# Kernel tuning notes

Hardware: AMD Instinct MI355X
Metric: run time of the kernel (lower is better)

## Reference

```python
import jax, jax.numpy as jnp
import numpy as np
import math

B, S, H, NH, NB = 2, 512, 128, 4, 2
D = H // NH
V_ITEMS, NCAT, NMETA, BAG, TSPAN = 50000, 1000, 16, 5, 256
EPS_EMB, EPS = 1e-5, 1e-8
NEG = -(2.0 ** 32) + 1.0


def _ln(x, g, b, eps):
    m = x.mean(-1, keepdims=True)
    v = ((x - m) ** 2).mean(-1, keepdims=True)
    return (x - m) / jnp.sqrt(v + eps) * g + b


def setup_inputs() -> dict:
    key = jax.random.key(0)
    ks = jax.random.split(key, 24)
    sc = 0.02
    inp = {}
    inp['input_ids'] = jax.random.randint(ks[0], (B, S), 0, V_ITEMS + 1)
    inp['metadata_seq'] = jax.random.normal(ks[1], (B, S, NMETA), jnp.float32)
    inp['category_seq'] = jax.random.randint(ks[2], (B, S, BAG), 0, NCAT + 1)
    inp['time_matrix'] = jax.random.randint(ks[3], (B, S, S), 0, TSPAN + 1)
    item = jax.random.normal(ks[4], (V_ITEMS + 1, H), jnp.float32) * sc
    inp['item_emb_w'] = item.at[0].set(0.0)  # padding_idx=0 cleared
    cat = jax.random.normal(ks[5], (NCAT + 1, H // 2), jnp.float32) * sc
    inp['cat_emb_w'] = cat.at[0].set(0.0)
    inp['num_W'] = jax.random.normal(ks[6], (H // 2, NMETA), jnp.float32) * sc
    inp['num_b'] = jnp.zeros((H // 2,), jnp.float32)
    inp['fusion_W'] = jax.random.normal(ks[7], (H, 2 * H), jnp.float32) * sc
    inp['fusion_b'] = jnp.zeros((H,), jnp.float32)
    inp['emb_ln_g'] = jnp.ones((H,), jnp.float32)
    inp['emb_ln_b'] = jnp.zeros((H,), jnp.float32)
    inp['pos_K_w'] = jax.random.normal(ks[8], (S, H), jnp.float32) * sc
    inp['pos_V_w'] = jax.random.normal(ks[9], (S, H), jnp.float32) * sc
    inp['time_K_w'] = jax.random.normal(ks[10], (TSPAN + 1, H), jnp.float32) * sc
    inp['time_V_w'] = jax.random.normal(ks[11], (TSPAN + 1, H), jnp.float32) * sc
    inp['attn_ln_g'] = jnp.ones((NB, H), jnp.float32)
    inp['attn_ln_b'] = jnp.zeros((NB, H), jnp.float32)
    inp['Q_W'] = jax.random.normal(ks[12], (NB, H, H), jnp.float32) * sc
    inp['Q_b'] = jnp.zeros((NB, H), jnp.float32)
    inp['K_W'] = jax.random.normal(ks[13], (NB, H, H), jnp.float32) * sc
    inp['K_b'] = jnp.zeros((NB, H), jnp.float32)
    inp['V_W'] = jax.random.normal(ks[14], (NB, H, H), jnp.float32) * sc
    inp['V_b'] = jnp.zeros((NB, H), jnp.float32)
    inp['fwd_ln_g'] = jnp.ones((NB, H), jnp.float32)
    inp['fwd_ln_b'] = jnp.zeros((NB, H), jnp.float32)
    inp['w1_W'] = jax.random.normal(ks[15], (NB, H, H), jnp.float32) * sc
    inp['w1_b'] = jnp.zeros((NB, H), jnp.float32)
    inp['w2_W'] = jax.random.normal(ks[16], (NB, H, H), jnp.float32) * sc
    inp['w2_b'] = jnp.zeros((NB, H), jnp.float32)
    inp['last_ln_g'] = jnp.ones((H,), jnp.float32)
    inp['last_ln_b'] = jnp.zeros((H,), jnp.float32)
    return inp


def reference(input_ids, metadata_seq, category_seq, time_matrix, item_emb_w,
              cat_emb_w, num_W, num_b, fusion_W, fusion_b, emb_ln_g, emb_ln_b,
              pos_K_w, pos_V_w, time_K_w, time_V_w, attn_ln_g, attn_ln_b,
              Q_W, Q_b, K_W, K_b, V_W, V_b, fwd_ln_g, fwd_ln_b,
              w1_W, w1_b, w2_W, w2_b, last_ln_g, last_ln_b):
    # ---- seq2vec ----
    item_v = item_emb_w[input_ids] * math.sqrt(H)            # [B,S,H]
    bag_mask = (category_seq != 0)                           # EmbeddingBag mean, padding_idx=0
    cat_e = cat_emb_w[category_seq] * bag_mask[..., None]    # [B,S,BAG,H/2]
    cat_v = cat_e.sum(-2) / jnp.maximum(bag_mask.sum(-1, keepdims=True), 1)
    num_v = metadata_seq @ num_W.T + num_b                   # [B,S,H/2]
    comb = jnp.concatenate([item_v, num_v, cat_v], axis=-1)  # [B,S,2H]
    vecs = _ln(comb @ fusion_W.T + fusion_b, emb_ln_g, emb_ln_b, EPS_EMB)

    # ---- vec2feats ----
    posK = pos_K_w.reshape(S, NH, D)
    posV = pos_V_w.reshape(S, NH, D)
    tK = time_K_w[time_matrix].reshape(B, S, S, NH, D)       # [B,S,S,h,d]
    tV = time_V_w[time_matrix].reshape(B, S, S, NH, D)
    timeline = (input_ids == 0)                              # [B,S]
    keep = (~timeline)[..., None].astype(vecs.dtype)
    vecs = vecs * keep
    causal = ~jnp.tril(jnp.ones((S, S), bool))               # mask where j > i
    inv_sqrt_d = 1.0 / math.sqrt(D)

    for i in range(NB):
        Qn = _ln(vecs, attn_ln_g[i], attn_ln_b[i], EPS)
        Q = (Qn @ Q_W[i].T + Q_b[i]).reshape(B, S, NH, D)
        K = (vecs @ K_W[i].T + K_b[i]).reshape(B, S, NH, D)
        V = (vecs @ V_W[i].T + V_b[i]).reshape(B, S, NH, D)
        aw = jnp.einsum('bihd,bjhd->bhij', Q, K)
        aw = aw + jnp.einsum('bihd,jhd->bhij', Q, posK)
        aw = aw + jnp.einsum('bijhd,bihd->bhij', tK, Q)
        aw = aw * inv_sqrt_d
        aw = jnp.where(timeline[:, None, :, None], NEG, aw)  # masks query rows (as in torch)
        aw = jnp.where(causal[None, None], NEG, aw)
        aw = jax.nn.softmax(aw, axis=-1)
        out = jnp.einsum('bhij,bjhd->bihd', aw, V)
        out = out + jnp.einsum('bhij,jhd->bihd', aw, posV)
        out = out + jnp.einsum('bhij,bijhd->bihd', aw, tV)
        out = out.reshape(B, S, H)
        vecs = Qn + out
        vecs = _ln(vecs, fwd_ln_g[i], fwd_ln_b[i], EPS)
        h1 = jax.nn.gelu(vecs @ w1_W[i].T + w1_b[i], approximate=False)
        vecs = vecs + (h1 @ w2_W[i].T + w2_b[i])
        vecs = vecs * keep

    return _ln(vecs, last_ln_g, last_ln_b, EPS)
```

## Files before the change

### kernel.cpp

```cpp
#include <hip/hip_runtime.h>
#include <math.h>

#define Bn 2
#define Sn 512
#define Hn 128
#define NHn 4
#define Dn 32
#define BAGn 5
#define NMETAn 16
#define ROWS 1024
#define NBn 2
#define Tt 257

#define NEGF (-4294967295.0f)
#define INV_SQRT_D 0.17677669529663687f
#define SQRT_H 11.313708498984761f
#define EPS_EMB 1e-5f
#define EPSF 1e-8f

#define OFF_QN    0
#define OFF_Q     131072
#define OFF_K     262144
#define OFF_V     393216
#define OFF_O     524288

static __device__ __forceinline__ float red64(float v) {
#pragma unroll
    for (int m = 1; m < 64; m <<= 1) v += __shfl_xor(v, m, 64);
    return v;
}
static __device__ __forceinline__ float red64max(float v) {
#pragma unroll
    for (int m = 1; m < 64; m <<= 1) v = fmaxf(v, __shfl_xor(v, m, 64));
    return v;
}
static __device__ __forceinline__ float dot4(float4 a, float4 b) {
    return a.x * b.x + a.y * b.y + a.z * b.z + a.w * b.w;
}
static __device__ __forceinline__ float red4(float v) {
    v += __shfl_xor(v, 1, 64);
    v += __shfl_xor(v, 2, 64);
    return v;
}

__global__ __launch_bounds__(256) void embed_qkv_kernel(
    const int* __restrict__ ids, const float* __restrict__ meta,
    const int* __restrict__ cats,
    const float* __restrict__ item_w, const float* __restrict__ cat_w,
    const float* __restrict__ numW, const float* __restrict__ numb,
    const float* __restrict__ fusW, const float* __restrict__ fusb,
    const float* __restrict__ elng, const float* __restrict__ elnb,
    const float* __restrict__ alng, const float* __restrict__ alnb,
    const float* __restrict__ QW, const float* __restrict__ Qb,
    const float* __restrict__ KW, const float* __restrict__ Kb,
    const float* __restrict__ VW, const float* __restrict__ Vb,
    const float* __restrict__ posK, const float* __restrict__ posV,
    float* __restrict__ Qn, float* __restrict__ Q,
    float* __restrict__ K, float* __restrict__ V)
{
    int r0 = blockIdx.x * 2, t = threadIdx.x;
    __shared__ __align__(16) float combs[512];
    __shared__ __align__(16) float xs[256];
    __shared__ __align__(16) float qs[256];
    __shared__ float wsum[8];
    __shared__ int idl[2];
    if (t < 2) idl[t] = ids[r0 + t];
    __syncthreads();
    { int r = t >> 7, c = t & 127; combs[r * 256 + c] = item_w[idl[r] * Hn + c] * SQRT_H; }
    if (t < 128) {
        int r = t >> 6, c = t & 63;
        const float4* m4 = (const float4*)(meta + (r0 + r) * NMETAn);
        const float4* w4 = (const float4*)(numW + c * NMETAn);
        float acc = numb[c];
#pragma unroll
        for (int j = 0; j < 4; ++j) acc += dot4(m4[j], w4[j]);
        combs[r * 256 + 128 + c] = acc;
    } else {
        int u = t - 128, r = u >> 6, c = u & 63;
        float ca = 0.f; int cnt = 0;
#pragma unroll
        for (int k2 = 0; k2 < BAGn; ++k2) {
            int cc2 = cats[(r0 + r) * BAGn + k2];
            if (cc2 != 0) { ca += cat_w[cc2 * 64 + c]; cnt++; }
        }
        combs[r * 256 + 192 + c] = ca / (float)(cnt > 0 ? cnt : 1);
    }
    __syncthreads();

    int q = t & 3, g = t >> 2;
#pragma unroll
    for (int p = 0; p < 2; ++p) {
        int h = p * 64 + g;
        const float4* w4 = (const float4*)(fusW + h * 256) + q;
        const float4* c0 = (const float4*)(combs) + q;
        const float4* c1 = (const float4*)(combs + 256) + q;
        float a0 = 0.f, a1 = 0.f;
#pragma unroll
        for (int j = 0; j < 16; ++j) {
            float4 w = w4[j * 4];
            a0 += dot4(c0[j * 4], w);
            a1 += dot4(c1[j * 4], w);
        }
        a0 = red4(a0); a1 = red4(a1);
        if (q == 0)      xs[h]       = a0 + fusb[h];
        else if (q == 1) xs[128 + h] = a1 + fusb[h];
    }
    __syncthreads();

    int w_ = t >> 6, row = w_ >> 1, l = t & 63, ch = ((w_ & 1) << 6) + l;
    float x = xs[row * 128 + ch];
    float s1 = red64(x);
    if (l == 0) wsum[w_] = s1;
    __syncthreads();
    float mean = (wsum[row * 2] + wsum[row * 2 + 1]) * (1.f / 128.f);
    float dlt = x - mean;
    float s2 = red64(dlt * dlt);
    if (l == 0) wsum[4 + w_] = s2;
    __syncthreads();
    float rstd = rsqrtf((wsum[4 + row * 2] + wsum[4 + row * 2 + 1]) * (1.f / 128.f) + EPS_EMB);
    float xv = dlt * rstd * elng[ch] + elnb[ch];
    xv = (idl[row] == 0) ? 0.f : xv;
    __syncthreads();
    xs[row * 128 + ch] = xv;
    __syncthreads();
    s1 = red64(xv);
    if (l == 0) wsum[w_] = s1;
    __syncthreads();
    mean = (wsum[row * 2] + wsum[row * 2 + 1]) * (1.f / 128.f);
    dlt = xv - mean;
    s2 = red64(dlt * dlt);
    if (l == 0) wsum[4 + w_] = s2;
    __syncthreads();
    rstd = rsqrtf((wsum[4 + row * 2] + wsum[4 + row * 2 + 1]) * (1.f / 128.f) + EPSF);
    float qn = dlt * rstd * alng[ch] + alnb[ch];
    qs[row * 128 + ch] = qn;
    Qn[(r0 + row) * 128 + ch] = qn;
    __syncthreads();

#pragma unroll
    for (int p = 0; p < 2; ++p) {
        int h = p * 64 + g;
        const float4* qw = (const float4*)(QW + h * 128) + q;
        const float4* kw = (const float4*)(KW + h * 128) + q;
        const float4* vw = (const float4*)(VW + h * 128) + q;
        const float4* s0p = (const float4*)(qs) + q;
        const float4* s1p = (const float4*)(qs + 128) + q;
        const float4* x0p = (const float4*)(xs) + q;
        const float4* x1p = (const float4*)(xs + 128) + q;
        float aq0 = 0, aq1 = 0, ak0 = 0, ak1 = 0, av0 = 0, av1 = 0;
#pragma unroll
        for (int j = 0; j < 8; ++j) {
            float4 wq = qw[j * 4], wk = kw[j * 4], wv = vw[j * 4];
            float4 u0 = s0p[j * 4], u1 = s1p[j * 4];
            float4 y0 = x0p[j * 4], y1 = x1p[j * 4];
            aq0 += dot4(u0, wq); aq1 += dot4(u1, wq);
            ak0 += dot4(y0, wk); ak1 += dot4(y1, wk);
            av0 += dot4(y0, wv); av1 += dot4(y1, wv);
        }
        aq0 = red4(aq0); aq1 = red4(aq1);
        ak0 = red4(ak0); ak1 = red4(ak1);
        av0 = red4(av0); av1 = red4(av1);
        if (q == 0) {
            int si = r0 & (Sn - 1);
            Q[r0 * Hn + h] = aq0 + Qb[h];
            K[r0 * Hn + h] = ak0 + Kb[h] + posK[si * Hn + h];
            V[r0 * Hn + h] = av0 + Vb[h] + posV[si * Hn + h];
        } else if (q == 1) {
            int si = (r0 + 1) & (Sn - 1);
            Q[(r0 + 1) * Hn + h] = aq1 + Qb[h];
            K[(r0 + 1) * Hn + h] = ak1 + Kb[h] + posK[si * Hn + h];
            V[(r0 + 1) * Hn + h] = av1 + Vb[h] + posV[si * Hn + h];
        }
    }
}

static __device__ __forceinline__ void attn_phase(
    int b, int h, int i0, int t,
    const int* __restrict__ ids, const int* __restrict__ tmat,
    const float* __restrict__ Q, const float* __restrict__ K,
    const float* __restrict__ V,
    const float* __restrict__ tKw, const float* __restrict__ tVw,
    float* __restrict__ O,
    float* Kt, float* Vt, float* Stile, int* trowT,
    float* QTl, float* ql, int* tlf)
{
    if (t < 4) tlf[t] = (ids[b * Sn + i0 + t] == 0) ? 1 : 0;
    if (t < 128) {
        int q_ = t >> 5, d = t & 31;
        ql[q_ * 33 + d] = Q[(b * Sn + i0 + q_) * Hn + h * 32 + d];
    }
    __syncthreads();

    for (int tt = t; tt < Tt; tt += 256) {
        const float4* tk4 = (const float4*)(tKw + tt * Hn + h * 32);
        float a0 = 0.f, a1 = 0.f, a2 = 0.f, a3 = 0.f;
#pragma unroll
        for (int dv = 0; dv < 8; ++dv) {
            float4 w4 = tk4[dv];
            int d = dv * 4;
            a0 += ql[d] * w4.x + ql[d + 1] * w4.y + ql[d + 2] * w4.z + ql[d + 3] * w4.w;
            a1 += ql[33 + d] * w4.x + ql[34 + d] * w4.y + ql[35 + d] * w4.z + ql[36 + d] * w4.w;
            a2 += ql[66 + d] * w4.x + ql[67 + d] * w4.y + ql[68 + d] * w4.z + ql[69 + d] * w4.w;
            a3 += ql[99 + d] * w4.x + ql[100 + d] * w4.y + ql[101 + d] * w4.z + ql[102 + d] * w4.w;
        }
        QTl[tt] = a0; QTl[260 + tt] = a1; QTl[520 + tt] = a2; QTl[780 + tt] = a3;
    }

    int tl_any = tlf[0] | tlf[1] | tlf[2] | tlf[3];
    int ntiles = tl_any ? 8 : ((i0 + 3) >> 6) + 1;

    int iq = t >> 6, jj = t & 63;
    int i_g = i0 + iq;
    int my_tl = tlf[iq];
    const int* trow = tmat + (b * Sn + i_g) * Sn;

    float qreg[32];
#pragma unroll
    for (int d = 0; d < 32; ++d) qreg[d] = ql[iq * 33 + d];

    int jq = jj >> 5, d = jj & 31;
    float m = -INFINITY, lsum = 0.f, acc = 0.f;

    for (int jt = 0; jt < ntiles; ++jt) {
        int j0 = jt * 64;
        __syncthreads();
        for (int f = t; f < 64 * 8; f += 256) {
            int jl = f >> 3, dv = f & 7;
            const float* src = K + (b * Sn + j0 + jl) * Hn + h * 32 + dv * 4;
            float4 w4 = *(const float4*)src;
            float* kd = &Kt[jl * 33 + dv * 4];
            kd[0] = w4.x; kd[1] = w4.y; kd[2] = w4.z; kd[3] = w4.w;
            float4 v4 = *(const float4*)(V + (b * Sn + j0 + jl) * Hn + h * 32 + dv * 4);
            float* vd = &Vt[jl * 33 + dv * 4];
            vd[0] = v4.x; vd[1] = v4.y; vd[2] = v4.z; vd[3] = v4.w;
        }
        __syncthreads();

        int active = my_tl || (j0 <= i_g);
        if (active) {
            int j = j0 + jj;
            float sv = NEGF;
            int tv = trow[j];
            if (!my_tl && j <= i_g) {
                float a = 0.f;
#pragma unroll
                for (int dd = 0; dd < 32; ++dd)
                    a += qreg[dd] * Kt[jj * 33 + dd];
                sv = (a + QTl[iq * 260 + tv]) * INV_SQRT_D;
            }
            float mt = red64max(sv);
            float mnew = fmaxf(m, mt);
            float alpha = expf(m - mnew);
            float p = expf(sv - mnew);
            lsum = lsum * alpha + red64(p);
            m = mnew;
            acc *= alpha;
            Stile[iq * 64 + jj] = p;
            trowT[iq * 64 + jj] = tv;
        }
        __syncthreads();
        if (active) {
            int base = jq * 32;
#pragma unroll 8
            for (int jl = base; jl < base + 32; ++jl) {
                float pp = Stile[iq * 64 + jl];
                int tv2 = trowT[iq * 64 + jl];
                acc += pp * (Vt[jl * 33 + d] + tVw[tv2 * Hn + h * 32 + d]);
            }
        }
    }

    float a2 = acc + __shfl_xor(acc, 32, 64);
    if (jj < 32)
        O[(b * Sn + i_g) * Hn + h * 32 + d] = a2 / lsum;
}

__global__ __launch_bounds__(256) void attn_kernel(
    const int* ids, const int* tmat,
    const float* Q, const float* K, const float* V,
    const float* tKw, const float* tVw, float* O)
{
    __shared__ float Kt[64 * 33];
    __shared__ float Vt[64 * 33];
    __shared__ float Stile[4 * 64];
    __shared__ int   trowT[4 * 64];
    __shared__ float QTl[4 * 260];
    __shared__ float ql[4 * 33];
    __shared__ int tlf[4];
    int blk = blockIdx.x, t = threadIdx.x;
    int bh = blk & 7;
    int s  = blk >> 3;
    int g = s >> 5, r = s & 31;
    int mm;
    if      (g == 0) mm = r;
    else if (g == 1) mm = 127 - r;
    else if (g == 2) mm = 32 + r;
    else             mm = 95 - r;
    int b = bh >> 2, h = bh & 3;
    attn_phase(b, h, mm * 4, t, ids, tmat, Q, K, V, tKw, tVw, O,
               Kt, Vt, Stile, trowT, QTl, ql, tlf);
}

__global__ __launch_bounds__(256) void ffn_qkv_kernel(
    const int* __restrict__ ids, float* __restrict__ Qn,
    const float* __restrict__ O,
    const float* __restrict__ flng, const float* __restrict__ flnb,
    const float* __restrict__ w1W, const float* __restrict__ w1b,
    const float* __restrict__ w2W, const float* __restrict__ w2b,
    const float* __restrict__ alng, const float* __restrict__ alnb,
    const float* __restrict__ QW, const float* __restrict__ Qb,
    const float* __restrict__ KW, const float* __restrict__ Kb,
    const float* __restrict__ VW, const float* __restrict__ Vb,
    const float* __restrict__ posK, const float* __restrict__ posV,
    float* __restrict__ Q, float* __restrict__ K, float* __restrict__ V,
    const float* __restrict__ llng, const float* __restrict__ llnb,
    float* __restrict__ out, int nb, int last)
{
    int r0 = blockIdx.x * 2, t = threadIdx.x;
    __shared__ __align__(16) float ys[256];
    __shared__ __align__(16) float h1s[256];
    __shared__ float wsum[8];
    int id0 = ids[r0], id1 = ids[r0 + 1];

    ys[t] = Qn[r0 * 128 + t] + O[r0 * 128 + t];
    __syncthreads();
    int w_ = t >> 6, row = w_ >> 1, l = t & 63, ch = ((w_ & 1) << 6) + l;
    float x = ys[row * 128 + ch];
    float s1 = red64(x);
    if (l == 0) wsum[w_] = s1;
    __syncthreads();
    float mean = (wsum[row * 2] + wsum[row * 2 + 1]) * (1.f / 128.f);
    float dlt = x - mean;
    float s2 = red64(dlt * dlt);
    if (l == 0) wsum[4 + w_] = s2;
    __syncthreads();
    float rstd = rsqrtf((wsum[4 + row * 2] + wsum[4 + row * 2 + 1]) * (1.f / 128.f) + EPSF);
    float yv = dlt * rstd * flng[nb * 128 + ch] + flnb[nb * 128 + ch];
    __syncthreads();
    ys[row * 128 + ch] = yv;
    __syncthreads();

    int q = t & 3, g = t >> 2;
#pragma unroll
    for (int p = 0; p < 2; ++p) {
        int h = p * 64 + g;
        const float4* w4 = (const float4*)(w1W + nb * 16384 + h * 128) + q;
        const float4* y0 = (const float4*)(ys) + q;
        const float4* y1 = (const float4*)(ys + 128) + q;
        float a0 = 0.f, a1 = 0.f;
#pragma unroll
        for (int j = 0; j < 8; ++j) {
            float4 w = w4[j * 4];
            a0 += dot4(y0[j * 4], w);
            a1 += dot4(y1[j * 4], w);
        }
        a0 = red4(a0); a1 = red4(a1);
        if (q == 0) {
            float v0 = a0 + w1b[nb * 128 + h];
            h1s[h] = 0.5f * v0 * (1.f + erff(v0 * 0.70710678118654752f));
        } else if (q == 1) {
            float v1 = a1 + w1b[nb * 128 + h];
            h1s[128 + h] = 0.5f * v1 * (1.f + erff(v1 * 0.70710678118654752f));
        }
    }
    __syncthreads();

    float z00, z01, z10, z11;
    {
        float zz[2][2];
#pragma unroll
        for (int p = 0; p < 2; ++p) {
            int h = p * 64 + g;
            const float4* w4 = (const float4*)(w2W + nb * 16384 + h * 128) + q;
            const float4* y0 = (const float4*)(h1s) + q;
            const float4* y1 = (const float4*)(h1s + 128) + q;
            float a0 = 0.f, a1 = 0.f;
#pragma unroll
            for (int j = 0; j < 8; ++j) {
                float4 w = w4[j * 4];
                a0 += dot4(y0[j * 4], w);
                a1 += dot4(y1[j * 4], w);
            }
            a0 = red4(a0); a1 = red4(a1);
            float b_ = w2b[nb * 128 + h];
            zz[p][0] = (id0 == 0) ? 0.f : (a0 + b_ + ys[h]);
            zz[p][1] = (id1 == 0) ? 0.f : (a1 + b_ + ys[128 + h]);
        }
        z00 = zz[0][0]; z10 = zz[1][0]; z01 = zz[0][1]; z11 = zz[1][1];
    }
    __syncthreads();
    if (q == 0)      { h1s[g] = z00;        h1s[64 + g] = z10; }
    else if (q == 1) { h1s[128 + g] = z01;  h1s[192 + g] = z11; }
    __syncthreads();

    if (last) {
        x = h1s[row * 128 + ch];
        s1 = red64(x);
        if (l == 0) wsum[w_] = s1;
        __syncthreads();
        mean = (wsum[row * 2] + wsum[row * 2 + 1]) * (1.f / 128.f);
        dlt = x - mean;
        s2 = red64(dlt * dlt);
        if (l == 0) wsum[4 + w_] = s2;
        __syncthreads();
        rstd = rsqrtf((wsum[4 + row * 2] + wsum[4 + row * 2 + 1]) * (1.f / 128.f) + EPSF);
        out[(r0 + row) * 128 + ch] = dlt * rstd * llng[ch] + llnb[ch];
        return;
    }

    int nq = nb + 1;
    x = h1s[row * 128 + ch];
    s1 = red64(x);
    if (l == 0) wsum[w_] = s1;
    __syncthreads();
    mean = (wsum[row * 2] + wsum[row * 2 + 1]) * (1.f / 128.f);
    dlt = x - mean;
    s2 = red64(dlt * dlt);
    if (l == 0) wsum[4 + w_] = s2;
    __syncthreads();
    rstd = rsqrtf((wsum[4 + row * 2] + wsum[4 + row * 2 + 1]) * (1.f / 128.f) + EPSF);
    float qn = dlt * rstd * alng[nq * 128 + ch] + alnb[nq * 128 + ch];
    __syncthreads();
    ys[row * 128 + ch] = qn;
    Qn[(r0 + row) * 128 + ch] = qn;
    __syncthreads();

#pragma unroll
    for (int p = 0; p < 2; ++p) {
        int h = p * 64 + g;
        const float4* qw = (const float4*)(QW + nq * 16384 + h * 128) + q;
        const float4* kw = (const float4*)(KW + nq * 16384 + h * 128) + q;
        const float4* vw = (const float4*)(VW + nq * 16384 + h * 128) + q;
        const float4* s0p = (const float4*)(ys) + q;
        const float4* s1p = (const float4*)(ys + 128) + q;
        const float4* x0p = (const float4*)(h1s) + q;
        const float4* x1p = (const float4*)(h1s + 128) + q;
        float aq0 = 0, aq1 = 0, ak0 = 0, ak1 = 0, av0 = 0, av1 = 0;
#pragma unroll
        for (int j = 0; j < 8; ++j) {
            float4 wq = qw[j * 4], wk = kw[j * 4], wv = vw[j * 4];
            float4 u0 = s0p[j * 4], u1 = s1p[j * 4];
            float4 y0 = x0p[j * 4], y1 = x1p[j * 4];
            aq0 += dot4(u0, wq); aq1 += dot4(u1, wq);
            ak0 += dot4(y0, wk); ak1 += dot4(y1, wk);
            av0 += dot4(y0, wv); av1 += dot4(y1, wv);
        }
        aq0 = red4(aq0); aq1 = red4(aq1);
        ak0 = red4(ak0); ak1 = red4(ak1);
        av0 = red4(av0); av1 = red4(av1);
        if (q == 0) {
            int si = r0 & (Sn - 1);
            Q[r0 * Hn + h] = aq0 + Qb[nq * 128 + h];
            K[r0 * Hn + h] = ak0 + Kb[nq * 128 + h] + posK[si * Hn + h];
            V[r0 * Hn + h] = av0 + Vb[nq * 128 + h] + posV[si * Hn + h];
        } else if (q == 1) {
            int si = (r0 + 1) & (Sn - 1);
            Q[(r0 + 1) * Hn + h] = aq1 + Qb[nq * 128 + h];
            K[(r0 + 1) * Hn + h] = ak1 + Kb[nq * 128 + h] + posK[si * Hn + h];
            V[(r0 + 1) * Hn + h] = av1 + Vb[nq * 128 + h] + posV[si * Hn + h];
        }
    }
}

extern "C" void kernel_launch(void* const* d_in, const int* in_sizes, int n_in,
                              void* d_out, int out_size, void* d_ws, size_t ws_size,
                              hipStream_t stream) {
    const int*   ids   = (const int*)  d_in[0];
    const float* meta  = (const float*)d_in[1];
    const int*   cats  = (const int*)  d_in[2];
    const int*   tmat  = (const int*)  d_in[3];
    const float* itemw = (const float*)d_in[4];
    const float* catw  = (const float*)d_in[5];
    const float* numW  = (const float*)d_in[6];
    const float* numb  = (const float*)d_in[7];
    const float* fusW  = (const float*)d_in[8];
    const float* fusb  = (const float*)d_in[9];
    const float* elng  = (const float*)d_in[10];
    const float* elnb  = (const float*)d_in[11];
    const float* posK  = (const float*)d_in[12];
    const float* posV  = (const float*)d_in[13];
    const float* tKw   = (const float*)d_in[14];
    const float* tVw   = (const float*)d_in[15];
    const float* alng  = (const float*)d_in[16];
    const float* alnb  = (const float*)d_in[17];
    const float* QW    = (const float*)d_in[18];
    const float* Qb    = (const float*)d_in[19];
    const float* KW    = (const float*)d_in[20];
    const float* Kb    = (const float*)d_in[21];
    const float* VW    = (const float*)d_in[22];
    const float* Vb    = (const float*)d_in[23];
    const float* flng  = (const float*)d_in[24];
    const float* flnb  = (const float*)d_in[25];
    const float* w1W   = (const float*)d_in[26];
    const float* w1b   = (const float*)d_in[27];
    const float* w2W   = (const float*)d_in[28];
    const float* w2b   = (const float*)d_in[29];
    const float* llng  = (const float*)d_in[30];
    const float* llnb  = (const float*)d_in[31];
    (void)in_sizes; (void)n_in; (void)out_size; (void)ws_size;

    float* ws = (float*)d_ws;
    float* Qnp = ws + OFF_QN;
    float* Qp  = ws + OFF_Q;
    float* Kp  = ws + OFF_K;
    float* Vp  = ws + OFF_V;
    float* Op  = ws + OFF_O;
    float* outp = (float*)d_out;

    embed_qkv_kernel<<<ROWS / 2, 256, 0, stream>>>(
        ids, meta, cats, itemw, catw, numW, numb, fusW, fusb, elng, elnb,
        alng, alnb, QW, Qb, KW, Kb, VW, Vb, posK, posV, Qnp, Qp, Kp, Vp);
    for (int nb = 0; nb < NBn; ++nb) {
        attn_kernel<<<1024, 256, 0, stream>>>(ids, tmat, Qp, Kp, Vp, tKw, tVw, Op);
        ffn_qkv_kernel<<<ROWS / 2, 256, 0, stream>>>(
            ids, Qnp, Op, flng, flnb, w1W, w1b, w2W, w2b,
            alng, alnb, QW, Qb, KW, Kb, VW, Vb, posK, posV,
            Qp, Kp, Vp, llng, llnb, outp, nb, (nb == NBn - 1) ? 1 : 0);
    }
}
```

Before: 229.0 us.

## Prefetch time matrix and time tables into cache; parallelize QT projection

The embedding kernel now reads the whole time matrix and both time embedding tables and throws the values away, so they sit in L2/MALL before the attention kernels run. An empty asm statement keeps the dead loads from being removed. The attention kernel's per-query time-key projection now splits each 32-wide dot product across 4 lanes with shuffle reductions, so all 256 threads share the 257 time buckets instead of one thread per bucket looping serially. The cost is extra memory traffic in the embedding kernel and some additional shuffle instructions.

```diff
diff --git a/kernel.cpp b/kernel.cpp
--- a/kernel.cpp
+++ b/kernel.cpp
@@ -55,6 +55,8 @@
     const float* __restrict__ KW, const float* __restrict__ Kb,
     const float* __restrict__ VW, const float* __restrict__ Vb,
     const float* __restrict__ posK, const float* __restrict__ posV,
+    const int* __restrict__ tmat, const float* __restrict__ tKw,
+    const float* __restrict__ tVw,
     float* __restrict__ Qn, float* __restrict__ Q,
     float* __restrict__ K, float* __restrict__ V)
 {
@@ -64,6 +66,20 @@
     __shared__ __align__(16) float qs[256];
     __shared__ float wsum[8];
     __shared__ int idl[2];
+
+    int pfi = 0; float pff = 0.f;
+    {
+        const int* tm = tmat + blockIdx.x * 1024;
+#pragma unroll
+        for (int j = 0; j < 4; ++j) pfi += tm[t + j * 256];
+        if (t < 64) {
+            int off = blockIdx.x * 64 + t;
+            pff = tKw[off] + tVw[off];
+        } else if (blockIdx.x == 0 && t < 192) {
+            pff = tKw[32704 + t] + tVw[32704 + t];
+        }
+    }
+
     if (t < 2) idl[t] = ids[r0 + t];
     __syncthreads();
     { int r = t >> 7, c = t & 127; combs[r * 256 + c] = item_w[idl[r] * Hn + c] * SQRT_H; }
@@ -85,6 +101,7 @@
         }
         combs[r * 256 + 192 + c] = ca / (float)(cnt > 0 ? cnt : 1);
     }
+    asm volatile("" :: "v"(pfi), "v"(pff));
     __syncthreads();
 
     int q = t & 3, g = t >> 2;
@@ -191,19 +208,48 @@
     }
     __syncthreads();
 
-    for (int tt = t; tt < Tt; tt += 256) {
-        const float4* tk4 = (const float4*)(tKw + tt * Hn + h * 32);
-        float a0 = 0.f, a1 = 0.f, a2 = 0.f, a3 = 0.f;
-#pragma unroll
-        for (int dv = 0; dv < 8; ++dv) {
-            float4 w4 = tk4[dv];
-            int d = dv * 4;
-            a0 += ql[d] * w4.x + ql[d + 1] * w4.y + ql[d + 2] * w4.z + ql[d + 3] * w4.w;
-            a1 += ql[33 + d] * w4.x + ql[34 + d] * w4.y + ql[35 + d] * w4.z + ql[36 + d] * w4.w;
-            a2 += ql[66 + d] * w4.x + ql[67 + d] * w4.y + ql[68 + d] * w4.z + ql[69 + d] * w4.w;
-            a3 += ql[99 + d] * w4.x + ql[100 + d] * w4.y + ql[101 + d] * w4.z + ql[102 + d] * w4.w;
-        }
-        QTl[tt] = a0; QTl[260 + tt] = a1; QTl[520 + tt] = a2; QTl[780 + tt] = a3;
+    {
+        int qq = t & 3, gg = t >> 2;
+#pragma unroll
+        for (int c = 0; c < 4; ++c) {
+            int tt = c * 64 + gg;
+            const float4* tk4 = (const float4*)(tKw + tt * Hn + h * 32);
+            float4 wA = tk4[qq];
+            float4 wB = tk4[qq + 4];
+            int dA = qq * 4, dB = 16 + qq * 4;
+            float a0 = ql[dA]*wA.x + ql[dA+1]*wA.y + ql[dA+2]*wA.z + ql[dA+3]*wA.w
+                     + ql[dB]*wB.x + ql[dB+1]*wB.y + ql[dB+2]*wB.z + ql[dB+3]*wB.w;
+            float a1 = ql[33+dA]*wA.x + ql[34+dA]*wA.y + ql[35+dA]*wA.z + ql[36+dA]*wA.w
+                     + ql[33+dB]*wB.x + ql[34+dB]*wB.y + ql[35+dB]*wB.z + ql[36+dB]*wB.w;
+            float a2 = ql[66+dA]*wA.x + ql[67+dA]*wA.y + ql[68+dA]*wA.z + ql[69+dA]*wA.w
+                     + ql[66+dB]*wB.x + ql[67+dB]*wB.y + ql[68+dB]*wB.z + ql[69+dB]*wB.w;
+            float a3 = ql[99+dA]*wA.x + ql[100+dA]*wA.y + ql[101+dA]*wA.z + ql[102+dA]*wA.w
+                     + ql[99+dB]*wB.x + ql[100+dB]*wB.y + ql[101+dB]*wB.z + ql[102+dB]*wB.w;
+            a0 = red4(a0); a1 = red4(a1); a2 = red4(a2); a3 = red4(a3);
+            if (qq == 0)      QTl[tt] = a0;
+            else if (qq == 1) QTl[260 + tt] = a1;
+            else if (qq == 2) QTl[520 + tt] = a2;
+            else              QTl[780 + tt] = a3;
+        }
+        if (t < 4) {
+            const float4* tk4 = (const float4*)(tKw + 256 * Hn + h * 32);
+            float4 wA = tk4[t];
+            float4 wB = tk4[t + 4];
+            int dA = t * 4, dB = 16 + t * 4;
+            float a0 = ql[dA]*wA.x + ql[dA+1]*wA.y + ql[dA+2]*wA.z + ql[dA+3]*wA.w
+                     + ql[dB]*wB.x + ql[dB+1]*wB.y + ql[dB+2]*wB.z + ql[dB+3]*wB.w;
+            float a1 = ql[33+dA]*wA.x + ql[34+dA]*wA.y + ql[35+dA]*wA.z + ql[36+dA]*wA.w
+                     + ql[33+dB]*wB.x + ql[34+dB]*wB.y + ql[35+dB]*wB.z + ql[36+dB]*wB.w;
+            float a2 = ql[66+dA]*wA.x + ql[67+dA]*wA.y + ql[68+dA]*wA.z + ql[69+dA]*wA.w
+                     + ql[66+dB]*wB.x + ql[67+dB]*wB.y + ql[68+dB]*wB.z + ql[69+dB]*wB.w;
+            float a3 = ql[99+dA]*wA.x + ql[100+dA]*wA.y + ql[101+dA]*wA.z + ql[102+dA]*wA.w
+                     + ql[99+dB]*wB.x + ql[100+dB]*wB.y + ql[101+dB]*wB.z + ql[102+dB]*wB.w;
+            a0 = red4(a0); a1 = red4(a1); a2 = red4(a2); a3 = red4(a3);
+            if (t == 0)      QTl[256] = a0;
+            else if (t == 1) QTl[516] = a1;
+            else if (t == 2) QTl[776] = a2;
+            else             QTl[1036] = a3;
+        }
     }
 
     int tl_any = tlf[0] | tlf[1] | tlf[2] | tlf[3];
@@ -509,7 +555,8 @@
 
     embed_qkv_kernel<<<ROWS / 2, 256, 0, stream>>>(
         ids, meta, cats, itemw, catw, numW, numb, fusW, fusb, elng, elnb,
-        alng, alnb, QW, Qb, KW, Kb, VW, Vb, posK, posV, Qnp, Qp, Kp, Vp);
+        alng, alnb, QW, Qb, KW, Kb, VW, Vb, posK, posV, tmat, tKw, tVw,
+        Qnp, Qp, Kp, Vp);
     for (int nb = 0; nb < NBn; ++nb) {
         attn_kernel<<<1024, 256, 0, stream>>>(ids, tmat, Qp, Kp, Vp, tKw, tVw, Op);
         ffn_qkv_kernel<<<ROWS / 2, 256, 0, stream>>>(
```

Result: faster. 224.2 us (-2.1%).

## Fuse attention with FFN/QKV per row pair and double-buffer K/V

Applied to the files above, without the earlier changes.

Attention and the following FFN/LayerNorm/next-QKV projection are merged into one kernel. Each block handles two query rows across all four heads, with 32-key tiles, 32-lane reductions, and V and tV read straight from global memory. K/V outputs now alternate between two workspace buffers, because other blocks still read the current K/V while the next ones are written. This drops the intermediate O buffer and two kernel launches. The embed kernel also touches time_matrix and the time embedding tables to warm the cache, at the cost of extra loads and fewer, heavier attention blocks.

```diff
diff --git a/kernel.cpp b/kernel.cpp
--- a/kernel.cpp
+++ b/kernel.cpp
@@ -20,18 +20,24 @@
 
 #define OFF_QN    0
 #define OFF_Q     131072
-#define OFF_K     262144
-#define OFF_V     393216
-#define OFF_O     524288
+#define OFF_K0    262144
+#define OFF_V0    393216
+#define OFF_K1    524288
+#define OFF_V1    655360
 
 static __device__ __forceinline__ float red64(float v) {
 #pragma unroll
     for (int m = 1; m < 64; m <<= 1) v += __shfl_xor(v, m, 64);
     return v;
 }
-static __device__ __forceinline__ float red64max(float v) {
-#pragma unroll
-    for (int m = 1; m < 64; m <<= 1) v = fmaxf(v, __shfl_xor(v, m, 64));
+static __device__ __forceinline__ float red32(float v) {
+#pragma unroll
+    for (int m = 1; m < 32; m <<= 1) v += __shfl_xor(v, m, 32);
+    return v;
+}
+static __device__ __forceinline__ float red32max(float v) {
+#pragma unroll
+    for (int m = 1; m < 32; m <<= 1) v = fmaxf(v, __shfl_xor(v, m, 32));
     return v;
 }
 static __device__ __forceinline__ float dot4(float4 a, float4 b) {
@@ -55,6 +61,8 @@
     const float* __restrict__ KW, const float* __restrict__ Kb,
     const float* __restrict__ VW, const float* __restrict__ Vb,
     const float* __restrict__ posK, const float* __restrict__ posV,
+    const int* __restrict__ tmat, const float* __restrict__ tKw,
+    const float* __restrict__ tVw,
     float* __restrict__ Qn, float* __restrict__ Q,
     float* __restrict__ K, float* __restrict__ V)
 {
@@ -64,6 +72,20 @@
     __shared__ __align__(16) float qs[256];
     __shared__ float wsum[8];
     __shared__ int idl[2];
+
+    int pfi = 0; float pff = 0.f;
+    {
+        const int* tm = tmat + blockIdx.x * 1024;
+#pragma unroll
+        for (int j = 0; j < 4; ++j) pfi += tm[t + j * 256];
+        if (t < 64) {
+            int off = blockIdx.x * 64 + t;
+            pff = tKw[off] + tVw[off];
+        } else if (blockIdx.x == 0 && t < 192) {
+            pff = tKw[32704 + t] + tVw[32704 + t];
+        }
+    }
+
     if (t < 2) idl[t] = ids[r0 + t];
     __syncthreads();
     { int r = t >> 7, c = t & 127; combs[r * 256 + c] = item_w[idl[r] * Hn + c] * SQRT_H; }
@@ -85,6 +107,7 @@
         }
         combs[r * 256 + 192 + c] = ca / (float)(cnt > 0 ? cnt : 1);
     }
+    asm volatile("" :: "v"(pfi), "v"(pff));
     __syncthreads();
 
     int q = t & 3, g = t >> 2;
@@ -174,136 +197,11 @@
     }
 }
 
-static __device__ __forceinline__ void attn_phase(
-    int b, int h, int i0, int t,
+__global__ __launch_bounds__(256) void attn_ffn_kernel(
     const int* __restrict__ ids, const int* __restrict__ tmat,
-    const float* __restrict__ Q, const float* __restrict__ K,
-    const float* __restrict__ V,
+    const float* Q, const float* K, const float* V,
     const float* __restrict__ tKw, const float* __restrict__ tVw,
-    float* __restrict__ O,
-    float* Kt, float* Vt, float* Stile, int* trowT,
-    float* QTl, float* ql, int* tlf)
-{
-    if (t < 4) tlf[t] = (ids[b * Sn + i0 + t] == 0) ? 1 : 0;
-    if (t < 128) {
-        int q_ = t >> 5, d = t & 31;
-        ql[q_ * 33 + d] = Q[(b * Sn + i0 + q_) * Hn + h * 32 + d];
-    }
-    __syncthreads();
-
-    for (int tt = t; tt < Tt; tt += 256) {
-        const float4* tk4 = (const float4*)(tKw + tt * Hn + h * 32);
-        float a0 = 0.f, a1 = 0.f, a2 = 0.f, a3 = 0.f;
-#pragma unroll
-        for (int dv = 0; dv < 8; ++dv) {
-            float4 w4 = tk4[dv];
-            int d = dv * 4;
-            a0 += ql[d] * w4.x + ql[d + 1] * w4.y + ql[d + 2] * w4.z + ql[d + 3] * w4.w;
-            a1 += ql[33 + d] * w4.x + ql[34 + d] * w4.y + ql[35 + d] * w4.z + ql[36 + d] * w4.w;
-            a2 += ql[66 + d] * w4.x + ql[67 + d] * w4.y + ql[68 + d] * w4.z + ql[69 + d] * w4.w;
-            a3 += ql[99 + d] * w4.x + ql[100 + d] * w4.y + ql[101 + d] * w4.z + ql[102 + d] * w4.w;
-        }
-        QTl[tt] = a0; QTl[260 + tt] = a1; QTl[520 + tt] = a2; QTl[780 + tt] = a3;
-    }
-
-    int tl_any = tlf[0] | tlf[1] | tlf[2] | tlf[3];
-    int ntiles = tl_any ? 8 : ((i0 + 3) >> 6) + 1;
-
-    int iq = t >> 6, jj = t & 63;
-    int i_g = i0 + iq;
-    int my_tl = tlf[iq];
-    const int* trow = tmat + (b * Sn + i_g) * Sn;
-
-    float qreg[32];
-#pragma unroll
-    for (int d = 0; d < 32; ++d) qreg[d] = ql[iq * 33 + d];
-
-    int jq = jj >> 5, d = jj & 31;
-    float m = -INFINITY, lsum = 0.f, acc = 0.f;
-
-    for (int jt = 0; jt < ntiles; ++jt) {
-        int j0 = jt * 64;
-        __syncthreads();
-        for (int f = t; f < 64 * 8; f += 256) {
-            int jl = f >> 3, dv = f & 7;
-            const float* src = K + (b * Sn + j0 + jl) * Hn + h * 32 + dv * 4;
-            float4 w4 = *(const float4*)src;
-            float* kd = &Kt[jl * 33 + dv * 4];
-            kd[0] = w4.x; kd[1] = w4.y; kd[2] = w4.z; kd[3] = w4.w;
-            float4 v4 = *(const float4*)(V + (b * Sn + j0 + jl) * Hn + h * 32 + dv * 4);
-            float* vd = &Vt[jl * 33 + dv * 4];
-            vd[0] = v4.x; vd[1] = v4.y; vd[2] = v4.z; vd[3] = v4.w;
-        }
-        __syncthreads();
-
-        int active = my_tl || (j0 <= i_g);
-        if (active) {
-            int j = j0 + jj;
-            float sv = NEGF;
-            int tv = trow[j];
-            if (!my_tl && j <= i_g) {
-                float a = 0.f;
-#pragma unroll
-                for (int dd = 0; dd < 32; ++dd)
-                    a += qreg[dd] * Kt[jj * 33 + dd];
-                sv = (a + QTl[iq * 260 + tv]) * INV_SQRT_D;
-            }
-            float mt = red64max(sv);
-            float mnew = fmaxf(m, mt);
-            float alpha = expf(m - mnew);
-            float p = expf(sv - mnew);
-            lsum = lsum * alpha + red64(p);
-            m = mnew;
-            acc *= alpha;
-            Stile[iq * 64 + jj] = p;
-            trowT[iq * 64 + jj] = tv;
-        }
-        __syncthreads();
-        if (active) {
-            int base = jq * 32;
-#pragma unroll 8
-            for (int jl = base; jl < base + 32; ++jl) {
-                float pp = Stile[iq * 64 + jl];
-                int tv2 = trowT[iq * 64 + jl];
-                acc += pp * (Vt[jl * 33 + d] + tVw[tv2 * Hn + h * 32 + d]);
-            }
-        }
-    }
-
-    float a2 = acc + __shfl_xor(acc, 32, 64);
-    if (jj < 32)
-        O[(b * Sn + i_g) * Hn + h * 32 + d] = a2 / lsum;
-}
-
-__global__ __launch_bounds__(256) void attn_kernel(
-    const int* ids, const int* tmat,
-    const float* Q, const float* K, const float* V,
-    const float* tKw, const float* tVw, float* O)
-{
-    __shared__ float Kt[64 * 33];
-    __shared__ float Vt[64 * 33];
-    __shared__ float Stile[4 * 64];
-    __shared__ int   trowT[4 * 64];
-    __shared__ float QTl[4 * 260];
-    __shared__ float ql[4 * 33];
-    __shared__ int tlf[4];
-    int blk = blockIdx.x, t = threadIdx.x;
-    int bh = blk & 7;
-    int s  = blk >> 3;
-    int g = s >> 5, r = s & 31;
-    int mm;
-    if      (g == 0) mm = r;
-    else if (g == 1) mm = 127 - r;
-    else if (g == 2) mm = 32 + r;
-    else             mm = 95 - r;
-    int b = bh >> 2, h = bh & 3;
-    attn_phase(b, h, mm * 4, t, ids, tmat, Q, K, V, tKw, tVw, O,
-               Kt, Vt, Stile, trowT, QTl, ql, tlf);
-}
-
-__global__ __launch_bounds__(256) void ffn_qkv_kernel(
-    const int* __restrict__ ids, float* __restrict__ Qn,
-    const float* __restrict__ O,
+    float* __restrict__ Qn,
     const float* __restrict__ flng, const float* __restrict__ flnb,
     const float* __restrict__ w1W, const float* __restrict__ w1b,
     const float* __restrict__ w2W, const float* __restrict__ w2b,
@@ -312,20 +210,132 @@
     const float* __restrict__ KW, const float* __restrict__ Kb,
     const float* __restrict__ VW, const float* __restrict__ Vb,
     const float* __restrict__ posK, const float* __restrict__ posV,
-    float* __restrict__ Q, float* __restrict__ K, float* __restrict__ V,
+    float* Qo, float* Ko, float* Vo,
     const float* __restrict__ llng, const float* __restrict__ llnb,
     float* __restrict__ out, int nb, int last)
 {
-    int r0 = blockIdx.x * 2, t = threadIdx.x;
-    __shared__ __align__(16) float ys[256];
-    __shared__ __align__(16) float h1s[256];
-    __shared__ float wsum[8];
+    __shared__ __align__(16) float sm[7722];
+    float* Kt    = sm;
+    float* QTl   = sm + 4608;
+    float* ql    = sm + 6688;
+    float* os    = sm + 6952;
+    float* Stile = sm + 7208;
+    int*   trowT = (int*)(sm + 7464);
+    int*   tlf   = (int*)(sm + 7720);
+
+    int blk = blockIdx.x, t = threadIdx.x;
+    int beta = blk & 1;
+    int m_ = blk >> 1;
+    int grp = (m_ < 128) ? m_ : 383 - m_;
+    int r0 = beta * Sn + grp * 2;
+
+    int w  = t >> 6;
+    int jj = t & 63;
+    int r  = jj >> 5;
+    int j  = jj & 31;
+
+    if (t < 2) tlf[t] = (ids[r0 + t] == 0) ? 1 : 0;
+    { int rr = t >> 7, d = t & 127; ql[rr * 132 + d] = Q[(r0 + rr) * Hn + d]; }
+    __syncthreads();
+
+    {
+        int q4 = t & 3, g4 = t >> 2;
+        const float4* ql0 = (const float4*)(ql);
+        const float4* ql1 = (const float4*)(ql + 132);
+#pragma unroll
+        for (int c = 0; c < 5; ++c) {
+            int tt = c * 64 + g4;
+            if (tt < Tt) {
+                const float4* tk = (const float4*)(tKw + tt * Hn);
+                float ah[4][2] = {{0.f,0.f},{0.f,0.f},{0.f,0.f},{0.f,0.f}};
+#pragma unroll
+                for (int cc = 0; cc < 8; ++cc) {
+                    int chn = cc * 4 + q4;
+                    float4 wv = tk[chn];
+                    ah[cc >> 1][0] += dot4(ql0[chn], wv);
+                    ah[cc >> 1][1] += dot4(ql1[chn], wv);
+                }
+#pragma unroll
+                for (int hh = 0; hh < 4; ++hh) {
+                    ah[hh][0] = red4(ah[hh][0]);
+                    ah[hh][1] = red4(ah[hh][1]);
+                }
+                if (q4 == 0)      { QTl[tt] = ah[0][0];        QTl[260 + tt] = ah[0][1]; }
+                else if (q4 == 1) { QTl[520 + tt] = ah[1][0];  QTl[780 + tt] = ah[1][1]; }
+                else if (q4 == 2) { QTl[1040 + tt] = ah[2][0]; QTl[1300 + tt] = ah[2][1]; }
+                else              { QTl[1560 + tt] = ah[3][0]; QTl[1820 + tt] = ah[3][1]; }
+            }
+        }
+    }
+
+    int tl_any = tlf[0] | tlf[1];
+    int my_tl = tlf[r];
+    int i_g = grp * 2 + r;
+    int ntiles = tl_any ? 16 : ((grp * 2 + 1) >> 5) + 1;
+    const int* trw = tmat + (size_t)(r0 + r) * Sn;
+
+    float4 qv[8];
+    {
+        const float4* qp = (const float4*)(ql + r * 132 + w * 32);
+#pragma unroll
+        for (int d = 0; d < 8; ++d) qv[d] = qp[d];
+    }
+
+    float msm = -INFINITY, lsum = 0.f, acc = 0.f;
+    const float* Vb_  = V + (size_t)(beta * Sn) * Hn + w * 32 + j;
+    const float* tVb_ = tVw + w * 32 + j;
+
+    for (int jt = 0; jt < ntiles; ++jt) {
+        int j0 = jt * 32;
+        __syncthreads();
+#pragma unroll
+        for (int it = 0; it < 4; ++it) {
+            int f = it * 256 + t;
+            int jl = f >> 5, chn = f & 31;
+            float4 kv = *(const float4*)(K + (size_t)(beta * Sn + j0 + jl) * Hn + chn * 4);
+            *(float4*)(Kt + (chn >> 3) * 1152 + jl * 36 + (chn & 7) * 4) = kv;
+        }
+        __syncthreads();
+
+        int key = j0 + j;
+        float sv = NEGF;
+        int tv = trw[key];
+        if (!my_tl && key <= i_g) {
+            const float4* kr = (const float4*)(Kt + w * 1152 + j * 36);
+            float a = 0.f;
+#pragma unroll
+            for (int k4 = 0; k4 < 8; ++k4) a += dot4(qv[k4], kr[k4]);
+            sv = (a + QTl[(w * 2 + r) * 260 + tv]) * INV_SQRT_D;
+        }
+        float mt = red32max(sv);
+        float mnew = fmaxf(msm, mt);
+        float alpha = expf(msm - mnew);
+        float p = expf(sv - mnew);
+        lsum = lsum * alpha + red32(p);
+        msm = mnew;
+        acc *= alpha;
+        Stile[w * 64 + r * 32 + j] = p;
+        trowT[w * 64 + r * 32 + j] = tv;
+#pragma unroll 8
+        for (int jl = 0; jl < 32; ++jl) {
+            float pp = Stile[w * 64 + r * 32 + jl];
+            int tv2 = trowT[w * 64 + r * 32 + jl];
+            acc += pp * (Vb_[(size_t)(j0 + jl) * Hn] + tVb_[(size_t)tv2 * Hn]);
+        }
+    }
+
+    os[r * 128 + w * 32 + j] = acc / lsum;
+    __syncthreads();
+
+    float* ys   = sm;
+    float* h1s  = sm + 256;
+    float* wsum = sm + 512;
     int id0 = ids[r0], id1 = ids[r0 + 1];
 
-    ys[t] = Qn[r0 * 128 + t] + O[r0 * 128 + t];
-    __syncthreads();
-    int w_ = t >> 6, row = w_ >> 1, l = t & 63, ch = ((w_ & 1) << 6) + l;
-    float x = ys[row * 128 + ch];
+    ys[t] = Qn[r0 * 128 + t] + os[t];
+    __syncthreads();
+    int w_ = t >> 6, row = w_ >> 1, l = t & 63, chl = ((w_ & 1) << 6) + l;
+    float x = ys[row * 128 + chl];
     float s1 = red64(x);
     if (l == 0) wsum[w_] = s1;
     __syncthreads();
@@ -335,9 +345,9 @@
     if (l == 0) wsum[4 + w_] = s2;
     __syncthreads();
     float rstd = rsqrtf((wsum[4 + row * 2] + wsum[4 + row * 2 + 1]) * (1.f / 128.f) + EPSF);
-    float yv = dlt * rstd * flng[nb * 128 + ch] + flnb[nb * 128 + ch];
-    __syncthreads();
-    ys[row * 128 + ch] = yv;
+    float yv = dlt * rstd * flng[nb * 128 + chl] + flnb[nb * 128 + chl];
+    __syncthreads();
+    ys[row * 128 + chl] = yv;
     __syncthreads();
 
     int q = t & 3, g = t >> 2;
@@ -349,10 +359,10 @@
         const float4* y1 = (const float4*)(ys + 128) + q;
         float a0 = 0.f, a1 = 0.f;
 #pragma unroll
-        for (int j = 0; j < 8; ++j) {
-            float4 w = w4[j * 4];
-            a0 += dot4(y0[j * 4], w);
-            a1 += dot4(y1[j * 4], w);
+        for (int jx = 0; jx < 8; ++jx) {
+            float4 w4v = w4[jx * 4];
+            a0 += dot4(y0[jx * 4], w4v);
+            a1 += dot4(y1[jx * 4], w4v);
         }
         a0 = red4(a0); a1 = red4(a1);
         if (q == 0) {
@@ -376,10 +386,10 @@
             const float4* y1 = (const float4*)(h1s + 128) + q;
             float a0 = 0.f, a1 = 0.f;
 #pragma unroll
-            for (int j = 0; j < 8; ++j) {
-                float4 w = w4[j * 4];
-                a0 += dot4(y0[j * 4], w);
-                a1 += dot4(y1[j * 4], w);
+            for (int jx = 0; jx < 8; ++jx) {
+                float4 w4v = w4[jx * 4];
+                a0 += dot4(y0[jx * 4], w4v);
+                a1 += dot4(y1[jx * 4], w4v);
             }
             a0 = red4(a0); a1 = red4(a1);
             float b_ = w2b[nb * 128 + h];
@@ -394,7 +404,7 @@
     __syncthreads();
 
     if (last) {
-        x = h1s[row * 128 + ch];
+        x = h1s[row * 128 + chl];
         s1 = red64(x);
         if (l == 0) wsum[w_] = s1;
         __syncthreads();
@@ -404,12 +414,12 @@
         if (l == 0) wsum[4 + w_] = s2;
         __syncthreads();
         rstd = rsqrtf((wsum[4 + row * 2] + wsum[4 + row * 2 + 1]) * (1.f / 128.f) + EPSF);
-        out[(r0 + row) * 128 + ch] = dlt * rstd * llng[ch] + llnb[ch];
+        out[(r0 + row) * 128 + chl] = dlt * rstd * llng[chl] + llnb[chl];
         return;
     }
 
     int nq = nb + 1;
-    x = h1s[row * 128 + ch];
+    x = h1s[row * 128 + chl];
     s1 = red64(x);
     if (l == 0) wsum[w_] = s1;
     __syncthreads();
@@ -419,10 +429,10 @@
     if (l == 0) wsum[4 + w_] = s2;
     __syncthreads();
     rstd = rsqrtf((wsum[4 + row * 2] + wsum[4 + row * 2 + 1]) * (1.f / 128.f) + EPSF);
-    float qn = dlt * rstd * alng[nq * 128 + ch] + alnb[nq * 128 + ch];
-    __syncthreads();
-    ys[row * 128 + ch] = qn;
-    Qn[(r0 + row) * 128 + ch] = qn;
+    float qn = dlt * rstd * alng[nq * 128 + chl] + alnb[nq * 128 + chl];
+    __syncthreads();
+    ys[row * 128 + chl] = qn;
+    Qn[(r0 + row) * 128 + chl] = qn;
     __syncthreads();
 
 #pragma unroll
@@ -437,10 +447,10 @@
         const float4* x1p = (const float4*)(h1s + 128) + q;
         float aq0 = 0, aq1 = 0, ak0 = 0, ak1 = 0, av0 = 0, av1 = 0;
 #pragma unroll
-        for (int j = 0; j < 8; ++j) {
-            float4 wq = qw[j * 4], wk = kw[j * 4], wv = vw[j * 4];
-            float4 u0 = s0p[j * 4], u1 = s1p[j * 4];
-            float4 y0 = x0p[j * 4], y1 = x1p[j * 4];
+        for (int jx = 0; jx < 8; ++jx) {
+            float4 wq = qw[jx * 4], wk = kw[jx * 4], wv = vw[jx * 4];
+            float4 u0 = s0p[jx * 4], u1 = s1p[jx * 4];
+            float4 y0 = x0p[jx * 4], y1 = x1p[jx * 4];
             aq0 += dot4(u0, wq); aq1 += dot4(u1, wq);
             ak0 += dot4(y0, wk); ak1 += dot4(y1, wk);
             av0 += dot4(y0, wv); av1 += dot4(y1, wv);
@@ -450,14 +460,14 @@
         av0 = red4(av0); av1 = red4(av1);
         if (q == 0) {
             int si = r0 & (Sn - 1);
-            Q[r0 * Hn + h] = aq0 + Qb[nq * 128 + h];
-            K[r0 * Hn + h] = ak0 + Kb[nq * 128 + h] + posK[si * Hn + h];
-            V[r0 * Hn + h] = av0 + Vb[nq * 128 + h] + posV[si * Hn + h];
+            Qo[r0 * Hn + h] = aq0 + Qb[nq * 128 + h];
+            Ko[r0 * Hn + h] = ak0 + Kb[nq * 128 + h] + posK[si * Hn + h];
+            Vo[r0 * Hn + h] = av0 + Vb[nq * 128 + h] + posV[si * Hn + h];
         } else if (q == 1) {
             int si = (r0 + 1) & (Sn - 1);
-            Q[(r0 + 1) * Hn + h] = aq1 + Qb[nq * 128 + h];
-            K[(r0 + 1) * Hn + h] = ak1 + Kb[nq * 128 + h] + posK[si * Hn + h];
-            V[(r0 + 1) * Hn + h] = av1 + Vb[nq * 128 + h] + posV[si * Hn + h];
+            Qo[(r0 + 1) * Hn + h] = aq1 + Qb[nq * 128 + h];
+            Ko[(r0 + 1) * Hn + h] = ak1 + Kb[nq * 128 + h] + posK[si * Hn + h];
+            Vo[(r0 + 1) * Hn + h] = av1 + Vb[nq * 128 + h] + posV[si * Hn + h];
         }
     }
 }
@@ -502,19 +512,24 @@
     float* ws = (float*)d_ws;
     float* Qnp = ws + OFF_QN;
     float* Qp  = ws + OFF_Q;
-    float* Kp  = ws + OFF_K;
-    float* Vp  = ws + OFF_V;
-    float* Op  = ws + OFF_O;
+    float* K0  = ws + OFF_K0;
+    float* V0  = ws + OFF_V0;
+    float* K1  = ws + OFF_K1;
+    float* V1  = ws + OFF_V1;
     float* outp = (float*)d_out;
 
     embed_qkv_kernel<<<ROWS / 2, 256, 0, stream>>>(
         ids, meta, cats, itemw, catw, numW, numb, fusW, fusb, elng, elnb,
-        alng, alnb, QW, Qb, KW, Kb, VW, Vb, posK, posV, Qnp, Qp, Kp, Vp);
-    for (int nb = 0; nb < NBn; ++nb) {
-        attn_kernel<<<1024, 256, 0, stream>>>(ids, tmat, Qp, Kp, Vp, tKw, tVw, Op);
-        ffn_qkv_kernel<<<ROWS / 2, 256, 0, stream>>>(
-            ids, Qnp, Op, flng, flnb, w1W, w1b, w2W, w2b,
-            alng, alnb, QW, Qb, KW, Kb, VW, Vb, posK, posV,
-            Qp, Kp, Vp, llng, llnb, outp, nb, (nb == NBn - 1) ? 1 : 0);
-    }
-}
+        alng, alnb, QW, Qb, KW, Kb, VW, Vb, posK, posV, tmat, tKw, tVw,
+        Qnp, Qp, K0, V0);
+    attn_ffn_kernel<<<512, 256, 0, stream>>>(
+        ids, tmat, Qp, K0, V0, tKw, tVw, Qnp,
+        flng, flnb, w1W, w1b, w2W, w2b, alng, alnb,
+        QW, Qb, KW, Kb, VW, Vb, posK, posV,
+        Qp, K1, V1, llng, llnb, outp, 0, 0);
+    attn_ffn_kernel<<<512, 256, 0, stream>>>(
+        ids, tmat, Qp, K1, V1, tKw, tVw, Qnp,
+        flng, flnb, w1W, w1b, w2W, w2b, alng, alnb,
+        QW, Qb, KW, Kb, VW, Vb, posK, posV,
+        Qp, K0, V0, llng, llnb, outp, 1, 1);
+}
```

Measured after the change: 264.2 us. 1.15x slower.
